# Performance work log

Measured on AMD Instinct MI355X. Metric: run time of the kernel, lower is better.

## Reference

```python
import jax, jax.numpy as jnp
import numpy as np

N = 50000          # nodes
E = 800000         # edges (avg degree 16)
F_NODE = 128
F_EDGE = 32
HID = 32
HEADS = 4
C1 = HID           # out channels per head, conv1
C2 = HID // 2      # out channels per head, conv2
N_CLASSES = 2


def _glorot(key, shape):
    s = jnp.sqrt(6.0 / (shape[0] + shape[1]))
    return jax.random.uniform(key, shape, jnp.float32, -s, s)


def setup_inputs() -> dict:
    key = jax.random.key(0)
    ks = jax.random.split(key, 32)
    inp = {}
    inp["x"] = jax.random.normal(ks[0], (N, F_NODE), jnp.float32)
    inp["edge_index"] = jax.random.randint(ks[1], (2, E), 0, N)
    inp["edge_attr"] = jax.random.normal(ks[2], (E, F_EDGE), jnp.float32)
    # conv1 params (TransformerConv: lin_query/key/value with bias, lin_edge no bias, lin_skip with bias)
    inp["Wq1"] = _glorot(ks[3], (F_NODE, HEADS * C1)); inp["bq1"] = jnp.zeros((HEADS * C1,), jnp.float32)
    inp["Wk1"] = _glorot(ks[4], (F_NODE, HEADS * C1)); inp["bk1"] = jnp.zeros((HEADS * C1,), jnp.float32)
    inp["Wv1"] = _glorot(ks[5], (F_NODE, HEADS * C1)); inp["bv1"] = jnp.zeros((HEADS * C1,), jnp.float32)
    inp["We1"] = _glorot(ks[6], (F_EDGE, HEADS * C1))
    inp["Ws1"] = _glorot(ks[7], (F_NODE, C1)); inp["bs1"] = jnp.zeros((C1,), jnp.float32)
    # conv2 params (input dim = C1 due to head averaging)
    inp["Wq2"] = _glorot(ks[8], (C1, HEADS * C2)); inp["bq2"] = jnp.zeros((HEADS * C2,), jnp.float32)
    inp["Wk2"] = _glorot(ks[9], (C1, HEADS * C2)); inp["bk2"] = jnp.zeros((HEADS * C2,), jnp.float32)
    inp["Wv2"] = _glorot(ks[10], (C1, HEADS * C2)); inp["bv2"] = jnp.zeros((HEADS * C2,), jnp.float32)
    inp["We2"] = _glorot(ks[11], (F_EDGE, HEADS * C2))
    inp["Ws2"] = _glorot(ks[12], (C1, C2)); inp["bs2"] = jnp.zeros((C2,), jnp.float32)
    # dense head
    inp["W3"] = _glorot(ks[13], (C2, HID)); inp["b3"] = jnp.zeros((HID,), jnp.float32)
    inp["W4"] = _glorot(ks[14], (HID, N_CLASSES)); inp["b4"] = jnp.zeros((N_CLASSES,), jnp.float32)
    return inp


def _tconv(x, src, dst, ea, Wq, bq, Wk, bk, Wv, bv, We, Ws, bs, heads, c):
    n = x.shape[0]
    # project on nodes, then gather per edge: [E, H, C]
    q = (x @ Wq + bq).reshape(n, heads, c)[dst]
    e = (ea @ We).reshape(-1, heads, c)
    k = (x @ Wk + bk).reshape(n, heads, c)[src] + e
    v = (x @ Wv + bv).reshape(n, heads, c)[src] + e
    logits = (q * k).sum(-1) / jnp.sqrt(jnp.float32(c))      # [E, H]
    m = jax.ops.segment_max(logits, dst, num_segments=n)      # per-target max
    p = jnp.exp(logits - m[dst])
    s = jax.ops.segment_sum(p, dst, num_segments=n)
    alpha = p / s[dst]                                        # edge softmax [E, H]
    agg = jax.ops.segment_sum(alpha[:, :, None] * v, dst, num_segments=n)  # [N, H, C]
    return agg.mean(axis=1) + x @ Ws + bs                     # head-average + root skip


def reference(x, edge_index, edge_attr,
              Wq1, bq1, Wk1, bk1, Wv1, bv1, We1, Ws1, bs1,
              Wq2, bq2, Wk2, bk2, Wv2, bv2, We2, Ws2, bs2,
              W3, b3, W4, b4):
    src, dst = edge_index[0], edge_index[1]
    h = jax.nn.relu(_tconv(x, src, dst, edge_attr, Wq1, bq1, Wk1, bk1, Wv1, bv1, We1, Ws1, bs1, HEADS, C1))
    h = jax.nn.relu(_tconv(h, src, dst, edge_attr, Wq2, bq2, Wk2, bk2, Wv2, bv2, We2, Ws2, bs2, HEADS, C2))
    h = jax.nn.relu(h @ W3 + b3)
    return h @ W4 + b4
```

## Files before the change

kernel.cpp:

```cpp
#include <hip/hip_runtime.h>
#include <hip/hip_bf16.h>


constexpr int NN = 50000;
constexpr int NE = 800000;

typedef __attribute__((ext_vector_type(8))) short short8v;
typedef __attribute__((ext_vector_type(4))) float f32x4;

__device__ __forceinline__ float bl(unsigned u) { return __uint_as_float(u << 16); }
__device__ __forceinline__ float bh(unsigned u) { return __uint_as_float(u & 0xffff0000u); }
__device__ __forceinline__ unsigned short bfbits(float v) {
  __hip_bfloat16 t = __float2bfloat16(v);
  return *(unsigned short*)&t;
}
__device__ __forceinline__ unsigned pk2(float a, float b) {
  return (unsigned)bfbits(a) | ((unsigned)bfbits(b) << 16);
}

template <int K, int HC, int C>
__global__ __launch_bounds__(256) void make_wqe_k(
    const float* __restrict__ Wq, const float* __restrict__ bq,
    const float* __restrict__ We, float* __restrict__ Wqe) {
  const int idx = blockIdx.x * 256 + threadIdx.x;
  if (idx >= (K + 1) * 128) return;
  const int r = idx >> 7;
  const int hf = idx & 127;
  const int h = hf >> 5, f = hf & 31;
  float acc = 0.f;
#pragma unroll
  for (int c = 0; c < C; ++c) {
    const float wv = We[f * HC + h * C + c];
    const float qv = (r < K) ? Wq[r * HC + h * C + c] : bq[h * C + c];
    acc = fmaf(qv, wv, acc);
  }
  Wqe[idx] = acc;
}

template <int K, int QN, int CS, int NOUT>
__global__ __launch_bounds__(256) void pack_w_k(
    const float* __restrict__ Wq, const float* __restrict__ bq,
    const float* __restrict__ Wk, const float* __restrict__ bk,
    const float* __restrict__ Wv, const float* __restrict__ bv,
    const float* __restrict__ Ws, const float* __restrict__ bs,
    const float* __restrict__ Wqe,
    unsigned short* __restrict__ WcatT, float* __restrict__ biasCat) {
  const int t = blockIdx.x * 256 + threadIdx.x;
  if (t >= NOUT * K) return;
  const int nc = t / K, k = t % K;
  float w = 0.f, bias = 0.f;
  if (nc < QN)                    { w = Wq[k * QN + nc];            bias = bq[nc]; }
  else if (nc < 2 * QN)           { w = Wk[k * QN + nc - QN];       bias = bk[nc - QN]; }
  else if (nc < 3 * QN)           { w = Wv[k * QN + nc - 2 * QN];   bias = bv[nc - 2 * QN]; }
  else if (nc < 3 * QN + 128)     { w = Wqe[k * 128 + nc - 3 * QN]; bias = Wqe[K * 128 + nc - 3 * QN]; }
  else if (nc < 3 * QN + 128 + CS){ w = Ws[k * CS + nc - 3 * QN - 128]; bias = bs[nc - 3 * QN - 128]; }
  WcatT[(size_t)nc * K + k] = bfbits(w);
  if (k == 0) biasCat[nc] = bias;
}

__global__ __launch_bounds__(256) void cvt_bf16_k(
    const float* __restrict__ in, unsigned short* __restrict__ out, int n4) {
  const int t = blockIdx.x * 256 + threadIdx.x;
  if (t >= n4) return;
  const float4 v = *(const float4*)&in[(size_t)t * 4];
  uint2 o = { pk2(v.x, v.y), pk2(v.z, v.w) };
  *(uint2*)&out[(size_t)t * 4] = o;
}

template <int K, int QN, int CS, int NOUT>
__global__ __launch_bounds__(256) void mfma_proj_k(
    const unsigned short* __restrict__ Ab, const unsigned short* __restrict__ WcatT,
    const float* __restrict__ biasCat, float* __restrict__ qO,
    unsigned short* __restrict__ kbO, unsigned short* __restrict__ vbO,
    float* __restrict__ qeO, float* __restrict__ skipO, int n) {
  constexpr int KP = K + 8;
  __shared__ __align__(16) unsigned short As[128 * KP];
  __shared__ __align__(16) unsigned short Bs[64 * KP];
  const int bi = blockIdx.x * 128;
  const int n0 = blockIdx.y * 64;
  const int tid = threadIdx.x;
  for (int idx = tid; idx < 128 * (K / 8); idx += 256) {
    const int r = idx / (K / 8), s = idx % (K / 8);
    uint4 val = {0, 0, 0, 0};
    if (bi + r < n) val = *(const uint4*)&Ab[(size_t)(bi + r) * K + s * 8];
    *(uint4*)&As[r * KP + s * 8] = val;
  }
  for (int idx = tid; idx < 64 * (K / 8); idx += 256) {
    const int r = idx / (K / 8), s = idx % (K / 8);
    *(uint4*)&Bs[r * KP + s * 8] = *(const uint4*)&WcatT[(size_t)(n0 + r) * K + s * 8];
  }
  __syncthreads();
  const int w = tid >> 6, lane = tid & 63;
  const int lm = lane & 15, lk = lane >> 4;
  f32x4 acc[2][4];
#pragma unroll
  for (int nt = 0; nt < 4; ++nt) {
    const float bv = biasCat[n0 + nt * 16 + lm];
    acc[0][nt] = {bv, bv, bv, bv};
    acc[1][nt] = {bv, bv, bv, bv};
  }
#pragma unroll
  for (int ks = 0; ks < K / 32; ++ks) {
    const short8v a0 = *(const short8v*)&As[(w * 32 + lm) * KP + ks * 32 + lk * 8];
    const short8v a1 = *(const short8v*)&As[(w * 32 + 16 + lm) * KP + ks * 32 + lk * 8];
#pragma unroll
    for (int nt = 0; nt < 4; ++nt) {
      const short8v b = *(const short8v*)&Bs[(nt * 16 + lm) * KP + ks * 32 + lk * 8];
      acc[0][nt] = __builtin_amdgcn_mfma_f32_16x16x32_bf16(a0, b, acc[0][nt], 0, 0, 0);
      acc[1][nt] = __builtin_amdgcn_mfma_f32_16x16x32_bf16(a1, b, acc[1][nt], 0, 0, 0);
    }
  }
#pragma unroll
  for (int mt = 0; mt < 2; ++mt)
#pragma unroll
    for (int nt = 0; nt < 4; ++nt)
#pragma unroll
      for (int r = 0; r < 4; ++r) {
        const int row = bi + w * 32 + mt * 16 + lk * 4 + r;
        if (row >= n) continue;
        const int c = n0 + nt * 16 + lm;
        const float val = acc[mt][nt][r];
        if (c < QN)                      qO[(size_t)row * QN + c] = val;
        else if (c < 2 * QN)             kbO[(size_t)row * QN + (c - QN)] = bfbits(val);
        else if (c < 3 * QN)             vbO[(size_t)row * QN + (c - 2 * QN)] = bfbits(val);
        else if (c < 3 * QN + 128)       qeO[(size_t)row * 128 + (c - 3 * QN)] = val;
        else if (c < 3 * QN + 128 + CS)  skipO[(size_t)row * CS + (c - 3 * QN - 128)] = val;
      }
}

__global__ __launch_bounds__(256) void hist_k(const int* __restrict__ dst,
                                              int* __restrict__ deg, int nE) {
  const int i = blockIdx.x * 256 + threadIdx.x;
  if (i < nE) atomicAdd(&deg[dst[i]], 1);
}

__global__ __launch_bounds__(1024) void scan_k(const int* __restrict__ deg,
                                               int* __restrict__ rowptr,
                                               int* __restrict__ cursor, int n) {
  __shared__ int part[1024];
  const int t = threadIdx.x;
  const int chunk = (n + 1023) / 1024;
  const int lo = t * chunk;
  const int hi = min(lo + chunk, n);
  int s = 0;
  for (int i = lo; i < hi; ++i) s += deg[i];
  part[t] = s;
  __syncthreads();
  for (int off = 1; off < 1024; off <<= 1) {
    int tmp = (t >= off) ? part[t - off] : 0;
    __syncthreads();
    part[t] += tmp;
    __syncthreads();
  }
  int base = (t == 0) ? 0 : part[t - 1];
  for (int i = lo; i < hi; ++i) {
    rowptr[i] = base;
    cursor[i] = base;
    base += deg[i];
  }
  if (t == 1023) rowptr[n] = part[1023];
}

__global__ __launch_bounds__(256) void scatter_k(
    const int* __restrict__ src, const int* __restrict__ dst,
    int* __restrict__ cursor, int* __restrict__ csr_src,
    int* __restrict__ csr_eid, int nE) {
  const int i = blockIdx.x * 256 + threadIdx.x;
  if (i < nE) {
    const int d = dst[i];
    const int pos = atomicAdd(&cursor[d], 1);
    csr_src[pos] = src[i];
    csr_eid[pos] = i;
  }
}

__global__ __launch_bounds__(256) void permute_ea_k(
    const float* __restrict__ ea, const int* __restrict__ csr_eid,
    unsigned* __restrict__ eab, int nE) {
  const int t = blockIdx.x * 256 + threadIdx.x;
  if (t >= (nE + 16) * 16) return;
  const int pos = t >> 4, fp = t & 15;
  if (pos >= nE) { eab[(size_t)pos * 16 + fp] = 0; return; }
  const int eid = csr_eid[pos];
  const float2 v = *(const float2*)&ea[(size_t)eid * 32 + 2 * fp];
  eab[(size_t)pos * 16 + fp] = pk2(v.x, v.y);
}

template <int HC, int C, bool FINAL>
__global__ __launch_bounds__(256, 4) void tconv_fused_k(
    const float* __restrict__ q, const unsigned short* __restrict__ kb,
    const unsigned short* __restrict__ vb, const float* __restrict__ qe,
    const unsigned* __restrict__ eab, const int* __restrict__ rowptr,
    const int* __restrict__ csr_src, const float* __restrict__ We,
    const float* __restrict__ skip, const float* __restrict__ W3,
    const float* __restrict__ b3, const float* __restrict__ W4,
    const float* __restrict__ b4, float* __restrict__ outF,
    unsigned* __restrict__ outB, int n) {
  int d = (blockIdx.x * 256 + threadIdx.x) >> 6;
  d = __builtin_amdgcn_readfirstlane(d);
  const int lane = threadIdx.x & 63;
  if (d >= n) return;
  constexpr int CPL = HC / 64;
  const int gl = lane & 15;
  const int ch0 = lane * CPL;

  float q0, q1 = 0.f;
  if constexpr (CPL == 2) {
    const float2 qv = *(const float2*)&q[(size_t)d * HC + ch0];
    q0 = qv.x; q1 = qv.y;
  } else {
    q0 = q[(size_t)d * HC + ch0];
  }
  const float2 qev = *(const float2*)&qe[(size_t)d * 128 + (lane >> 4) * 32 + 2 * gl];
  const float inv = rsqrtf((float)C);

  float m = -INFINITY, sden = 0.f;
  float acc0 = 0.f, acc1 = 0.f, pea0 = 0.f, pea1 = 0.f;
  const int p0 = __builtin_amdgcn_readfirstlane(rowptr[d]);
  const int p1 = __builtin_amdgcn_readfirstlane(rowptr[d + 1]);

  for (int base = p0; base < p1; base += 16) {
    const int cnt = min(16, p1 - base);
    int sn[16];
#pragma unroll
    for (int j = 0; j < 16; ++j) {
      const int s = csr_src[base + j];
      sn[j] = ((unsigned)s < (unsigned)n) ? s : 0;
    }
    unsigned kw[16], vw[16], eu[16];
#pragma unroll
    for (int j = 0; j < 16; ++j) {
      if constexpr (CPL == 2) {
        kw[j] = *(const unsigned*)&kb[(size_t)sn[j] * HC + ch0];
        vw[j] = *(const unsigned*)&vb[(size_t)sn[j] * HC + ch0];
      } else {
        kw[j] = kb[(size_t)sn[j] * HC + ch0];
        vw[j] = vb[(size_t)sn[j] * HC + ch0];
      }
    }
#pragma unroll
    for (int j = 0; j < 16; ++j) eu[j] = eab[(size_t)(base + j) * 16 + gl];

    float l_l = -INFINITY;
#pragma unroll
    for (int j = 0; j < 16; ++j) {
      float dot;
      if constexpr (CPL == 2) {
        dot = q0 * bl(kw[j]) + q1 * bh(kw[j]);
      } else {
        dot = q0 * __uint_as_float(kw[j] << 16);
      }
      dot = fmaf(qev.x, bl(eu[j]), dot);
      dot = fmaf(qev.y, bh(eu[j]), dot);
#pragma unroll
      for (int off = 1; off < 16; off <<= 1) dot += __shfl_xor(dot, off, 16);
      l_l = (gl == j && j < cnt) ? dot * inv : l_l;
    }
    float cmax = l_l;
#pragma unroll
    for (int off = 1; off < 16; off <<= 1) cmax = fmaxf(cmax, __shfl_xor(cmax, off, 16));
    const float newm = fmaxf(m, cmax);
    const float scale = __expf(m - newm);
    const float p_l = __expf(l_l - newm);
    float csum = p_l;
#pragma unroll
    for (int off = 1; off < 16; off <<= 1) csum += __shfl_xor(csum, off, 16);
    sden = sden * scale + csum;
    acc0 *= scale; acc1 *= scale; pea0 *= scale; pea1 *= scale;
    m = newm;
#pragma unroll
    for (int j = 0; j < 16; ++j) {
      const float pj = __shfl(p_l, j, 16);
      if constexpr (CPL == 2) {
        acc0 = fmaf(pj, bl(vw[j]), acc0);
        acc1 = fmaf(pj, bh(vw[j]), acc1);
      } else {
        acc0 = fmaf(pj, __uint_as_float(vw[j] << 16), acc0);
      }
      pea0 = fmaf(pj, bl(eu[j]), pea0);
      pea1 = fmaf(pj, bh(eu[j]), pea1);
    }
  }

  const float rs = (sden > 0.f) ? 1.f / sden : 0.f;
  acc0 *= rs; acc1 *= rs; pea0 *= rs; pea1 *= rs;

  float cor0 = 0.f, cor1 = 0.f;
#pragma unroll
  for (int ff = 0; ff < 16; ++ff) {
    const float pf0 = __shfl(pea0, ff, 16);
    const float pf1 = __shfl(pea1, ff, 16);
    if constexpr (CPL == 2) {
      const float2 w0 = *(const float2*)&We[(2 * ff) * HC + ch0];
      const float2 w1 = *(const float2*)&We[(2 * ff + 1) * HC + ch0];
      cor0 = fmaf(pf0, w0.x, cor0); cor0 = fmaf(pf1, w1.x, cor0);
      cor1 = fmaf(pf0, w0.y, cor1); cor1 = fmaf(pf1, w1.y, cor1);
    } else {
      cor0 = fmaf(pf0, We[(2 * ff) * HC + ch0], cor0);
      cor0 = fmaf(pf1, We[(2 * ff + 1) * HC + ch0], cor0);
    }
  }
  acc0 += cor0; acc1 += cor1;

  acc0 += __shfl_xor(acc0, 16); acc0 += __shfl_xor(acc0, 32);
  if constexpr (CPL == 2) { acc1 += __shfl_xor(acc1, 16); acc1 += __shfl_xor(acc1, 32); }

  if constexpr (!FINAL) {
    if (lane < 16) {
      const int c0 = 2 * lane;
      const float v0 = fmaxf(acc0 * 0.25f + skip[(size_t)d * 32 + c0], 0.f);
      const float v1 = fmaxf(acc1 * 0.25f + skip[(size_t)d * 32 + c0 + 1], 0.f);
      outB[(size_t)d * 16 + lane] = pk2(v0, v1);
    }
  } else {
    const int c = lane & 15;
    const float h2 = fmaxf(acc0 * 0.25f + skip[(size_t)d * 16 + c], 0.f);
    const int j = lane & 31;
    float t3 = b3[j];
#pragma unroll
    for (int cc = 0; cc < 16; ++cc)
      t3 = fmaf(__shfl(h2, cc), W3[cc * 32 + j], t3);
    t3 = fmaxf(t3, 0.f);
    float o0 = t3 * W4[j * 2 + 0];
    float o1 = t3 * W4[j * 2 + 1];
#pragma unroll
    for (int off = 1; off < 32; off <<= 1) {
      o0 += __shfl_xor(o0, off);
      o1 += __shfl_xor(o1, off);
    }
    if (lane == 0) {
      outF[(size_t)d * 2 + 0] = o0 + b4[0];
      outF[(size_t)d * 2 + 1] = o1 + b4[1];
    }
  }
}

extern "C" void kernel_launch(void* const* d_in, const int* in_sizes, int n_in,
                              void* d_out, int out_size, void* d_ws, size_t ws_size,
                              hipStream_t stream) {
  const float* x   = (const float*)d_in[0];
  const int*   ei  = (const int*)d_in[1];
  const float* ea  = (const float*)d_in[2];
  const float* Wq1 = (const float*)d_in[3];  const float* bq1 = (const float*)d_in[4];
  const float* Wk1 = (const float*)d_in[5];  const float* bk1 = (const float*)d_in[6];
  const float* Wv1 = (const float*)d_in[7];  const float* bv1 = (const float*)d_in[8];
  const float* We1 = (const float*)d_in[9];
  const float* Ws1 = (const float*)d_in[10]; const float* bs1 = (const float*)d_in[11];
  const float* Wq2 = (const float*)d_in[12]; const float* bq2 = (const float*)d_in[13];
  const float* Wk2 = (const float*)d_in[14]; const float* bk2 = (const float*)d_in[15];
  const float* Wv2 = (const float*)d_in[16]; const float* bv2 = (const float*)d_in[17];
  const float* We2 = (const float*)d_in[18];
  const float* Ws2 = (const float*)d_in[19]; const float* bs2 = (const float*)d_in[20];
  const float* W3  = (const float*)d_in[21]; const float* b3  = (const float*)d_in[22];
  const float* W4  = (const float*)d_in[23]; const float* b4  = (const float*)d_in[24];
  const int* src = ei;
  const int* dst = ei + NE;

  float* wsf  = (float*)d_ws;
  float* q    = wsf;
  float* qe   = q + (size_t)NN * 128;
  float* skip = qe + (size_t)NN * 128;
  unsigned* h1b = (unsigned*)(skip + (size_t)NN * 32);
  float* Wqe  = (float*)(h1b + (size_t)NN * 16);
  float* biasCat = Wqe + 129 * 128;
  unsigned short* WcatT = (unsigned short*)(biasCat + 576);
  unsigned short* xb = WcatT + 576 * 128;
  unsigned short* kb = xb + (size_t)NN * 128;
  unsigned short* vb = kb + (size_t)NN * 128;
  unsigned* eab = (unsigned*)(vb + (size_t)NN * 128);
  int* deg     = (int*)(eab + (size_t)(NE + 16) * 16);
  int* rowptr  = deg + NN;
  int* cursor  = rowptr + NN + 1;
  int* csr_src = cursor + NN;
  int* csr_eid = csr_src + NE + 16;

  const int edgeGrid = (NE + 255) / 256;
  const int aggGrid  = (NN + 3) / 4;
  const int projRows = (NN + 127) / 128;

  hipMemsetAsync(deg, 0, (size_t)NN * sizeof(int), stream);
  hist_k<<<edgeGrid, 256, 0, stream>>>(dst, deg, NE);
  scan_k<<<1, 1024, 0, stream>>>(deg, rowptr, cursor, NN);
  scatter_k<<<edgeGrid, 256, 0, stream>>>(src, dst, cursor, csr_src, csr_eid, NE);
  permute_ea_k<<<((NE + 16) * 16 + 255) / 256, 256, 0, stream>>>(ea, csr_eid, eab, NE);

  make_wqe_k<128,128,32><<<(129*128+255)/256,256,0,stream>>>(Wq1, bq1, We1, Wqe);
  pack_w_k<128,128,32,576><<<(576*128+255)/256,256,0,stream>>>(
      Wq1, bq1, Wk1, bk1, Wv1, bv1, Ws1, bs1, Wqe, WcatT, biasCat);
  cvt_bf16_k<<<(NN*32+255)/256,256,0,stream>>>(x, xb, NN * 32);
  {
    dim3 grid(projRows, 9);
    mfma_proj_k<128,128,32,576><<<grid,256,0,stream>>>(
        xb, WcatT, biasCat, q, kb, vb, qe, skip, NN);
  }
  tconv_fused_k<128,32,false><<<aggGrid,256,0,stream>>>(
      q, kb, vb, qe, eab, rowptr, csr_src, We1, skip,
      nullptr, nullptr, nullptr, nullptr, nullptr, h1b, NN);

  make_wqe_k<32,64,16><<<(33*128+255)/256,256,0,stream>>>(Wq2, bq2, We2, Wqe);
  pack_w_k<32,64,16,384><<<(384*32+255)/256,256,0,stream>>>(
      Wq2, bq2, Wk2, bk2, Wv2, bv2, Ws2, bs2, Wqe, WcatT, biasCat);
  {
    dim3 grid(projRows, 6);
    mfma_proj_k<32,64,16,384><<<grid,256,0,stream>>>(
        (const unsigned short*)h1b, WcatT, biasCat, q, kb, vb, qe, skip, NN);
  }
  tconv_fused_k<64,16,true><<<aggGrid,256,0,stream>>>(
      q, kb, vb, qe, eab, rowptr, csr_src, We2, skip,
      W3, b3, W4, b4, (float*)d_out, nullptr, NN);
}
```

Baseline: 766.3 us.

## Double-buffer edge gathers, store q/qe in bf16, reuse A tile across column tiles

The aggregation loop now loads the next 16-edge chunk's source indices, K/V rows and edge attributes into a second register set while computing the current chunk, so gather latency can overlap the softmax math. The projection kernel keeps its A tile in shared memory and loops over three 64-column weight tiles per block instead of launching one block per tile, which cuts redundant A loads. q and qe are written and read as bf16 instead of fp32, halving their traffic at some precision cost. Double buffering doubles register use in a kernel bounded at 4 waves per SIMD, so it risks spills or lower occupancy.

```diff
diff --git a/kernel.cpp b/kernel.cpp
--- a/kernel.cpp
+++ b/kernel.cpp
@@ -70,14 +70,13 @@
 template <int K, int QN, int CS, int NOUT>
 __global__ __launch_bounds__(256) void mfma_proj_k(
     const unsigned short* __restrict__ Ab, const unsigned short* __restrict__ WcatT,
-    const float* __restrict__ biasCat, float* __restrict__ qO,
+    const float* __restrict__ biasCat, unsigned short* __restrict__ qO,
     unsigned short* __restrict__ kbO, unsigned short* __restrict__ vbO,
-    float* __restrict__ qeO, float* __restrict__ skipO, int n) {
+    unsigned short* __restrict__ qeO, float* __restrict__ skipO, int n) {
   constexpr int KP = K + 8;
   __shared__ __align__(16) unsigned short As[128 * KP];
   __shared__ __align__(16) unsigned short Bs[64 * KP];
   const int bi = blockIdx.x * 128;
-  const int n0 = blockIdx.y * 64;
   const int tid = threadIdx.x;
   for (int idx = tid; idx < 128 * (K / 8); idx += 256) {
     const int r = idx / (K / 8), s = idx % (K / 8);
@@ -85,47 +84,52 @@
     if (bi + r < n) val = *(const uint4*)&Ab[(size_t)(bi + r) * K + s * 8];
     *(uint4*)&As[r * KP + s * 8] = val;
   }
-  for (int idx = tid; idx < 64 * (K / 8); idx += 256) {
-    const int r = idx / (K / 8), s = idx % (K / 8);
-    *(uint4*)&Bs[r * KP + s * 8] = *(const uint4*)&WcatT[(size_t)(n0 + r) * K + s * 8];
-  }
-  __syncthreads();
   const int w = tid >> 6, lane = tid & 63;
   const int lm = lane & 15, lk = lane >> 4;
-  f32x4 acc[2][4];
-#pragma unroll
-  for (int nt = 0; nt < 4; ++nt) {
-    const float bv = biasCat[n0 + nt * 16 + lm];
-    acc[0][nt] = {bv, bv, bv, bv};
-    acc[1][nt] = {bv, bv, bv, bv};
-  }
-#pragma unroll
-  for (int ks = 0; ks < K / 32; ++ks) {
-    const short8v a0 = *(const short8v*)&As[(w * 32 + lm) * KP + ks * 32 + lk * 8];
-    const short8v a1 = *(const short8v*)&As[(w * 32 + 16 + lm) * KP + ks * 32 + lk * 8];
+#pragma unroll
+  for (int t = 0; t < 3; ++t) {
+    const int n0 = (blockIdx.y * 3 + t) * 64;
+    __syncthreads();
+    for (int idx = tid; idx < 64 * (K / 8); idx += 256) {
+      const int r = idx / (K / 8), s = idx % (K / 8);
+      *(uint4*)&Bs[r * KP + s * 8] = *(const uint4*)&WcatT[(size_t)(n0 + r) * K + s * 8];
+    }
+    __syncthreads();
+    f32x4 acc[2][4];
 #pragma unroll
     for (int nt = 0; nt < 4; ++nt) {
-      const short8v b = *(const short8v*)&Bs[(nt * 16 + lm) * KP + ks * 32 + lk * 8];
-      acc[0][nt] = __builtin_amdgcn_mfma_f32_16x16x32_bf16(a0, b, acc[0][nt], 0, 0, 0);
-      acc[1][nt] = __builtin_amdgcn_mfma_f32_16x16x32_bf16(a1, b, acc[1][nt], 0, 0, 0);
-    }
-  }
-#pragma unroll
-  for (int mt = 0; mt < 2; ++mt)
-#pragma unroll
-    for (int nt = 0; nt < 4; ++nt)
-#pragma unroll
-      for (int r = 0; r < 4; ++r) {
-        const int row = bi + w * 32 + mt * 16 + lk * 4 + r;
-        if (row >= n) continue;
-        const int c = n0 + nt * 16 + lm;
-        const float val = acc[mt][nt][r];
-        if (c < QN)                      qO[(size_t)row * QN + c] = val;
-        else if (c < 2 * QN)             kbO[(size_t)row * QN + (c - QN)] = bfbits(val);
-        else if (c < 3 * QN)             vbO[(size_t)row * QN + (c - 2 * QN)] = bfbits(val);
-        else if (c < 3 * QN + 128)       qeO[(size_t)row * 128 + (c - 3 * QN)] = val;
-        else if (c < 3 * QN + 128 + CS)  skipO[(size_t)row * CS + (c - 3 * QN - 128)] = val;
+      const float bv = biasCat[n0 + nt * 16 + lm];
+      acc[0][nt] = {bv, bv, bv, bv};
+      acc[1][nt] = {bv, bv, bv, bv};
+    }
+#pragma unroll
+    for (int ks = 0; ks < K / 32; ++ks) {
+      const short8v a0 = *(const short8v*)&As[(w * 32 + lm) * KP + ks * 32 + lk * 8];
+      const short8v a1 = *(const short8v*)&As[(w * 32 + 16 + lm) * KP + ks * 32 + lk * 8];
+#pragma unroll
+      for (int nt = 0; nt < 4; ++nt) {
+        const short8v b = *(const short8v*)&Bs[(nt * 16 + lm) * KP + ks * 32 + lk * 8];
+        acc[0][nt] = __builtin_amdgcn_mfma_f32_16x16x32_bf16(a0, b, acc[0][nt], 0, 0, 0);
+        acc[1][nt] = __builtin_amdgcn_mfma_f32_16x16x32_bf16(a1, b, acc[1][nt], 0, 0, 0);
       }
+    }
+#pragma unroll
+    for (int mt = 0; mt < 2; ++mt)
+#pragma unroll
+      for (int nt = 0; nt < 4; ++nt)
+#pragma unroll
+        for (int r = 0; r < 4; ++r) {
+          const int row = bi + w * 32 + mt * 16 + lk * 4 + r;
+          if (row >= n) continue;
+          const int c = n0 + nt * 16 + lm;
+          const float val = acc[mt][nt][r];
+          if (c < QN)                      qO[(size_t)row * QN + c] = bfbits(val);
+          else if (c < 2 * QN)             kbO[(size_t)row * QN + (c - QN)] = bfbits(val);
+          else if (c < 3 * QN)             vbO[(size_t)row * QN + (c - 2 * QN)] = bfbits(val);
+          else if (c < 3 * QN + 128)       qeO[(size_t)row * 128 + (c - 3 * QN)] = bfbits(val);
+          else if (c < 3 * QN + 128 + CS)  skipO[(size_t)row * CS + (c - 3 * QN - 128)] = val;
+        }
+  }
 }
 
 __global__ __launch_bounds__(256) void hist_k(const int* __restrict__ dst,
@@ -186,10 +190,73 @@
   eab[(size_t)pos * 16 + fp] = pk2(v.x, v.y);
 }
 
+#define TC_LOAD(kw, vw, eu, sn, bse)                                          \
+  {                                                                           \
+    _Pragma("unroll")                                                         \
+    for (int j = 0; j < 16; ++j) {                                            \
+      int s_ = __builtin_amdgcn_readfirstlane(csr_src[(bse) + j]);            \
+      sn[j] = ((unsigned)s_ < (unsigned)n) ? s_ : 0;                          \
+    }                                                                         \
+    _Pragma("unroll")                                                         \
+    for (int j = 0; j < 16; ++j) {                                            \
+      if constexpr (CPL == 2) {                                               \
+        kw[j] = *(const unsigned*)&kb[(size_t)sn[j] * HC + ch0];              \
+        vw[j] = *(const unsigned*)&vb[(size_t)sn[j] * HC + ch0];              \
+      } else {                                                                \
+        kw[j] = kb[(size_t)sn[j] * HC + ch0];                                 \
+        vw[j] = vb[(size_t)sn[j] * HC + ch0];                                 \
+      }                                                                       \
+    }                                                                         \
+    _Pragma("unroll")                                                         \
+    for (int j = 0; j < 16; ++j) eu[j] = eab[(size_t)((bse) + j) * 16 + gl];  \
+  }
+
+#define TC_COMPUTE(kw, vw, eu, bse)                                           \
+  {                                                                           \
+    const int cnt = min(16, p1 - (bse));                                      \
+    float l_l = -INFINITY;                                                    \
+    _Pragma("unroll")                                                         \
+    for (int j = 0; j < 16; ++j) {                                            \
+      float dot;                                                              \
+      if constexpr (CPL == 2) dot = q0 * bl(kw[j]) + q1 * bh(kw[j]);          \
+      else dot = q0 * __uint_as_float(kw[j] << 16);                           \
+      dot = fmaf(qx, bl(eu[j]), dot);                                         \
+      dot = fmaf(qy, bh(eu[j]), dot);                                         \
+      _Pragma("unroll")                                                       \
+      for (int off = 1; off < 16; off <<= 1) dot += __shfl_xor(dot, off, 16); \
+      l_l = (gl == j && j < cnt) ? dot * inv : l_l;                           \
+    }                                                                         \
+    float cmax = l_l;                                                         \
+    _Pragma("unroll")                                                         \
+    for (int off = 1; off < 16; off <<= 1)                                    \
+      cmax = fmaxf(cmax, __shfl_xor(cmax, off, 16));                          \
+    const float newm = fmaxf(m, cmax);                                        \
+    const float scale = __expf(m - newm);                                     \
+    const float p_l = __expf(l_l - newm);                                     \
+    float csum = p_l;                                                         \
+    _Pragma("unroll")                                                         \
+    for (int off = 1; off < 16; off <<= 1) csum += __shfl_xor(csum, off, 16); \
+    sden = sden * scale + csum;                                               \
+    acc0 *= scale; acc1 *= scale; pea0 *= scale; pea1 *= scale;               \
+    m = newm;                                                                 \
+    _Pragma("unroll")                                                         \
+    for (int j = 0; j < 16; ++j) {                                            \
+      const float pj = __shfl(p_l, j, 16);                                    \
+      if constexpr (CPL == 2) {                                               \
+        acc0 = fmaf(pj, bl(vw[j]), acc0);                                     \
+        acc1 = fmaf(pj, bh(vw[j]), acc1);                                     \
+      } else {                                                                \
+        acc0 = fmaf(pj, __uint_as_float(vw[j] << 16), acc0);                  \
+      }                                                                       \
+      pea0 = fmaf(pj, bl(eu[j]), pea0);                                       \
+      pea1 = fmaf(pj, bh(eu[j]), pea1);                                       \
+    }                                                                         \
+  }
+
 template <int HC, int C, bool FINAL>
 __global__ __launch_bounds__(256, 4) void tconv_fused_k(
-    const float* __restrict__ q, const unsigned short* __restrict__ kb,
-    const unsigned short* __restrict__ vb, const float* __restrict__ qe,
+    const unsigned short* __restrict__ qb, const unsigned short* __restrict__ kb,
+    const unsigned short* __restrict__ vb, const unsigned short* __restrict__ qe16,
     const unsigned* __restrict__ eab, const int* __restrict__ rowptr,
     const int* __restrict__ csr_src, const float* __restrict__ We,
     const float* __restrict__ skip, const float* __restrict__ W3,
@@ -206,12 +273,13 @@
 
   float q0, q1 = 0.f;
   if constexpr (CPL == 2) {
-    const float2 qv = *(const float2*)&q[(size_t)d * HC + ch0];
-    q0 = qv.x; q1 = qv.y;
+    const unsigned qw = *(const unsigned*)&qb[(size_t)d * HC + ch0];
+    q0 = bl(qw); q1 = bh(qw);
   } else {
-    q0 = q[(size_t)d * HC + ch0];
-  }
-  const float2 qev = *(const float2*)&qe[(size_t)d * 128 + (lane >> 4) * 32 + 2 * gl];
+    q0 = __uint_as_float(((unsigned)qb[(size_t)d * HC + ch0]) << 16);
+  }
+  const unsigned qev = *(const unsigned*)&qe16[(size_t)d * 128 + (lane >> 4) * 32 + 2 * gl];
+  const float qx = bl(qev), qy = bh(qev);
   const float inv = rsqrtf((float)C);
 
   float m = -INFINITY, sden = 0.f;
@@ -219,66 +287,22 @@
   const int p0 = __builtin_amdgcn_readfirstlane(rowptr[d]);
   const int p1 = __builtin_amdgcn_readfirstlane(rowptr[d + 1]);
 
-  for (int base = p0; base < p1; base += 16) {
-    const int cnt = min(16, p1 - base);
-    int sn[16];
-#pragma unroll
-    for (int j = 0; j < 16; ++j) {
-      const int s = csr_src[base + j];
-      sn[j] = ((unsigned)s < (unsigned)n) ? s : 0;
-    }
-    unsigned kw[16], vw[16], eu[16];
-#pragma unroll
-    for (int j = 0; j < 16; ++j) {
-      if constexpr (CPL == 2) {
-        kw[j] = *(const unsigned*)&kb[(size_t)sn[j] * HC + ch0];
-        vw[j] = *(const unsigned*)&vb[(size_t)sn[j] * HC + ch0];
-      } else {
-        kw[j] = kb[(size_t)sn[j] * HC + ch0];
-        vw[j] = vb[(size_t)sn[j] * HC + ch0];
-      }
-    }
-#pragma unroll
-    for (int j = 0; j < 16; ++j) eu[j] = eab[(size_t)(base + j) * 16 + gl];
-
-    float l_l = -INFINITY;
-#pragma unroll
-    for (int j = 0; j < 16; ++j) {
-      float dot;
-      if constexpr (CPL == 2) {
-        dot = q0 * bl(kw[j]) + q1 * bh(kw[j]);
-      } else {
-        dot = q0 * __uint_as_float(kw[j] << 16);
-      }
-      dot = fmaf(qev.x, bl(eu[j]), dot);
-      dot = fmaf(qev.y, bh(eu[j]), dot);
-#pragma unroll
-      for (int off = 1; off < 16; off <<= 1) dot += __shfl_xor(dot, off, 16);
-      l_l = (gl == j && j < cnt) ? dot * inv : l_l;
-    }
-    float cmax = l_l;
-#pragma unroll
-    for (int off = 1; off < 16; off <<= 1) cmax = fmaxf(cmax, __shfl_xor(cmax, off, 16));
-    const float newm = fmaxf(m, cmax);
-    const float scale = __expf(m - newm);
-    const float p_l = __expf(l_l - newm);
-    float csum = p_l;
-#pragma unroll
-    for (int off = 1; off < 16; off <<= 1) csum += __shfl_xor(csum, off, 16);
-    sden = sden * scale + csum;
-    acc0 *= scale; acc1 *= scale; pea0 *= scale; pea1 *= scale;
-    m = newm;
-#pragma unroll
-    for (int j = 0; j < 16; ++j) {
-      const float pj = __shfl(p_l, j, 16);
-      if constexpr (CPL == 2) {
-        acc0 = fmaf(pj, bl(vw[j]), acc0);
-        acc1 = fmaf(pj, bh(vw[j]), acc1);
-      } else {
-        acc0 = fmaf(pj, __uint_as_float(vw[j] << 16), acc0);
-      }
-      pea0 = fmaf(pj, bl(eu[j]), pea0);
-      pea1 = fmaf(pj, bh(eu[j]), pea1);
+  if (p0 < p1) {
+    unsigned kwA[16], vwA[16], euA[16]; int snA[16];
+    unsigned kwB[16], vwB[16], euB[16]; int snB[16];
+    int base = p0;
+    TC_LOAD(kwA, vwA, euA, snA, base);
+    while (true) {
+      int nb = base + 16;
+      if (nb < p1) TC_LOAD(kwB, vwB, euB, snB, nb);
+      TC_COMPUTE(kwA, vwA, euA, base);
+      base = nb;
+      if (base >= p1) break;
+      nb = base + 16;
+      if (nb < p1) TC_LOAD(kwA, vwA, euA, snA, nb);
+      TC_COMPUTE(kwB, vwB, euB, base);
+      base = nb;
+      if (base >= p1) break;
     }
   }
 
@@ -357,13 +381,13 @@
   const int* dst = ei + NE;
 
   float* wsf  = (float*)d_ws;
-  float* q    = wsf;
-  float* qe   = q + (size_t)NN * 128;
-  float* skip = qe + (size_t)NN * 128;
-  unsigned* h1b = (unsigned*)(skip + (size_t)NN * 32);
-  float* Wqe  = (float*)(h1b + (size_t)NN * 16);
+  float* skip = wsf;
+  float* Wqe  = skip + (size_t)NN * 32;
   float* biasCat = Wqe + 129 * 128;
-  unsigned short* WcatT = (unsigned short*)(biasCat + 576);
+  unsigned* h1b = (unsigned*)(biasCat + 576);
+  unsigned short* qb = (unsigned short*)(h1b + (size_t)NN * 16);
+  unsigned short* qe16 = qb + (size_t)NN * 128;
+  unsigned short* WcatT = qe16 + (size_t)NN * 128;
   unsigned short* xb = WcatT + 576 * 128;
   unsigned short* kb = xb + (size_t)NN * 128;
   unsigned short* vb = kb + (size_t)NN * 128;
@@ -389,23 +413,23 @@
       Wq1, bq1, Wk1, bk1, Wv1, bv1, Ws1, bs1, Wqe, WcatT, biasCat);
   cvt_bf16_k<<<(NN*32+255)/256,256,0,stream>>>(x, xb, NN * 32);
   {
-    dim3 grid(projRows, 9);
+    dim3 grid(projRows, 3);
     mfma_proj_k<128,128,32,576><<<grid,256,0,stream>>>(
-        xb, WcatT, biasCat, q, kb, vb, qe, skip, NN);
+        xb, WcatT, biasCat, qb, kb, vb, qe16, skip, NN);
   }
   tconv_fused_k<128,32,false><<<aggGrid,256,0,stream>>>(
-      q, kb, vb, qe, eab, rowptr, csr_src, We1, skip,
+      qb, kb, vb, qe16, eab, rowptr, csr_src, We1, skip,
       nullptr, nullptr, nullptr, nullptr, nullptr, h1b, NN);
 
   make_wqe_k<32,64,16><<<(33*128+255)/256,256,0,stream>>>(Wq2, bq2, We2, Wqe);
   pack_w_k<32,64,16,384><<<(384*32+255)/256,256,0,stream>>>(
       Wq2, bq2, Wk2, bk2, Wv2, bv2, Ws2, bs2, Wqe, WcatT, biasCat);
   {
-    dim3 grid(projRows, 6);
+    dim3 grid(projRows, 2);
     mfma_proj_k<32,64,16,384><<<grid,256,0,stream>>>(
-        (const unsigned short*)h1b, WcatT, biasCat, q, kb, vb, qe, skip, NN);
+        (const unsigned short*)h1b, WcatT, biasCat, qb, kb, vb, qe16, skip, NN);
   }
   tconv_fused_k<64,16,true><<<aggGrid,256,0,stream>>>(
-      q, kb, vb, qe, eab, rowptr, csr_src, We2, skip,
+      qb, kb, vb, qe16, eab, rowptr, csr_src, We2, skip,
       W3, b3, W4, b4, (float*)d_out, nullptr, NN);
 }
```

After: 1.155 ms. 1.51x slower.
